# Optimization experiments

Hardware: AMD Instinct MI355X
Metric: run time of the kernel (lower is better)

## Reference

```python
import jax, jax.numpy as jnp
import numpy as np

N_USERS, N_ITEMS, N_GENRES = 31360, 6807, 18
TOTAL = N_USERS + N_ITEMS + N_GENRES          # 38185
OFFSET = TOTAL - N_GENRES                      # 38167
D = 16                                         # embedding_dim
B = 524288                                     # batch
MLP_DIMS = [64, 32, 16]
IN_DIM = 3 * D                                 # field_num * embedding_dim


def setup_inputs() -> dict:
    key = jax.random.key(0)
    ks = jax.random.split(key, 14)
    user = jax.random.randint(ks[0], (B, 1), 0, N_USERS)
    item = N_USERS + jax.random.randint(ks[1], (B, 1), 0, N_ITEMS)
    x_onehot = jnp.concatenate([user, item], axis=1)            # [B,2] global ids
    multi_hot = jax.random.randint(ks[2], (B, N_GENRES), 0, 2)  # [B,18] 0/1 mask
    s = 0.05
    emb_table = s * jax.random.normal(ks[3], (TOTAL, D), jnp.float32)
    fc_table = s * jax.random.normal(ks[4], (TOTAL, 1), jnp.float32)
    W1 = s * jax.random.normal(ks[5], (IN_DIM, MLP_DIMS[0]), jnp.float32)
    b1 = jnp.zeros((MLP_DIMS[0],), jnp.float32)
    W2 = s * jax.random.normal(ks[6], (MLP_DIMS[0], MLP_DIMS[1]), jnp.float32)
    b2 = jnp.zeros((MLP_DIMS[1],), jnp.float32)
    W3 = s * jax.random.normal(ks[7], (MLP_DIMS[1], MLP_DIMS[2]), jnp.float32)
    b3 = jnp.zeros((MLP_DIMS[2],), jnp.float32)
    W4 = s * jax.random.normal(ks[8], (MLP_DIMS[2], 1), jnp.float32)
    b4 = jnp.zeros((1,), jnp.float32)
    bias = jnp.zeros((1,), jnp.float32)
    return {"x_onehot": x_onehot, "multi_hot": multi_hot,
            "emb_table": emb_table, "fc_table": fc_table,
            "W1": W1, "b1": b1, "W2": W2, "b2": b2,
            "W3": W3, "b3": b3, "W4": W4, "b4": b4, "bias": bias}


def reference(x_onehot, multi_hot, emb_table, fc_table,
              W1, b1, W2, b2, W3, b3, W4, b4, bias):
    mh = multi_hot.astype(emb_table.dtype)                      # [B,18]
    # ragged multi-hot sum == mask @ genre slice of table (EmbeddingBag sum)
    embed_mh = mh @ emb_table[OFFSET:]                          # [B,D]
    embed_x = jnp.concatenate(
        [emb_table[x_onehot], embed_mh[:, None, :]], axis=1)    # [B,3,D]
    fc_mh = mh @ fc_table[OFFSET:]                              # [B,1]
    fc_x = jnp.concatenate(
        [fc_table[x_onehot], fc_mh[:, None, :]], axis=1)        # [B,3,1]
    # FM second-order term
    sum_e = embed_x.sum(axis=1)                                 # [B,D]
    fm_y = bias + fc_x.sum(axis=1) + 0.5 * jnp.sum(
        sum_e ** 2 - (embed_x ** 2).sum(axis=1), axis=1, keepdims=True)  # [B,1]
    # MLP (dropout inactive at inference)
    h = embed_x.reshape(embed_x.shape[0], -1)                   # [B,48]
    h = jax.nn.relu(h @ W1 + b1)
    h = jax.nn.relu(h @ W2 + b2)
    h = jax.nn.relu(h @ W3 + b3)
    mlp_y = h @ W4 + b4                                         # [B,1]
    return jax.nn.sigmoid(fm_y[:, 0] + mlp_y[:, 0])             # [B]
```

## Files before the change

### kernel.cpp

```cpp
#include <hip/hip_runtime.h>
#include <hip/hip_bf16.h>

namespace {

constexpr int kBatch  = 524288;
constexpr int kD      = 16;
constexpr int kOffset = 38167;
constexpr int kNG     = 18;

constexpr int W1B0   = 0;
constexpr int W2B0   = 8192;
constexpr int W3B0   = 12288;
constexpr int GB0    = 13312;
constexpr int WBYTES = 14336;

typedef __attribute__((ext_vector_type(8))) short short8;
typedef __attribute__((ext_vector_type(4))) float f32x4;

__device__ __forceinline__ unsigned short f2bf(float f) {
    return __builtin_bit_cast(unsigned short, __float2bfloat16(f));
}
__device__ __forceinline__ unsigned pk2(float a, float b) {
    return (unsigned)f2bf(a) | ((unsigned)f2bf(b) << 16);
}
__device__ __forceinline__ float bf2f(unsigned short s) {
    union { unsigned u; float f; } v; v.u = ((unsigned)s) << 16;
    return v.f;
}

__global__ void prep_weights(const float* __restrict__ emb,
                             const float* __restrict__ W1,
                             const float* __restrict__ W2,
                             const float* __restrict__ W3,
                             unsigned short* __restrict__ wimg)
{
    const int t = (int)threadIdx.x;
    for (int i = t; i < WBYTES / 2; i += 256) wimg[i] = 0;
    __syncthreads();
    for (int i = t; i < 48 * 64; i += 256) {
        int k = i >> 6, n = i & 63;
        int byte = W1B0 + n * 128 + ((k * 2) ^ ((n & 7) << 4));
        wimg[byte >> 1] = f2bf(W1[k * 64 + n]);
    }
    for (int i = t; i < 64 * 32; i += 256) {
        int k = i >> 5, n = i & 31;
        int byte = W2B0 + n * 128 + ((k * 2) ^ ((n & 7) << 4));
        wimg[byte >> 1] = f2bf(W2[k * 32 + n]);
    }
    for (int i = t; i < 32 * 16; i += 256) {
        int k = i >> 4, n = i & 15;
        int byte = W3B0 + n * 64 + ((k * 2) ^ ((n & 3) << 4));
        wimg[byte >> 1] = f2bf(W3[k * 16 + n]);
    }
    for (int i = t; i < 512; i += 256) {
        int c = i >> 5, r = i & 31, g = r >> 3, j = r & 7;
        int kg = 8 * g + j;
        wimg[(GB0 >> 1) + (4 * c + g) * 8 + j] =
            (kg < kNG) ? f2bf(emb[(size_t)(kOffset + kg) * kD + c]) : (unsigned short)0;
    }
}

__global__ __launch_bounds__(256, 3) void deepfm_fwd(
    const int*   __restrict__ x_onehot,
    const int*   __restrict__ multi_hot,
    const float* __restrict__ emb,
    const float* __restrict__ fc,
    const unsigned short* __restrict__ wimg,
    const float* __restrict__ b1,
    const float* __restrict__ b2,
    const float* __restrict__ b3,
    const float* __restrict__ W4,
    const float* __restrict__ b4,
    const float* __restrict__ bias,
    float*       __restrict__ out)
{
    __shared__ alignas(16) unsigned short s_w[WBYTES / 2];
    __shared__ alignas(16) unsigned short s_act[4 * 4096];

    const int t = (int)threadIdx.x;

    {
        const uint4* src = reinterpret_cast<const uint4*>(wimg);
        uint4*       dst = reinterpret_cast<uint4*>(s_w);
        #pragma unroll
        for (int q = 0; q < 4; ++q) {
            const int idx = t + 256 * q;
            if (idx < WBYTES / 16) dst[idx] = src[idx];
        }
    }

    const int i    = (int)blockIdx.x * 256 + t;
    const int lane = t & 63;
    const int w    = t >> 6;
    const int c    = lane & 15, g = lane >> 4;
    char* __restrict__ awc = (char*)(s_act + w * 4096);
    const char* __restrict__ swc = (const char*)s_w;

    const int l7 = lane & 7;
    const int sb = lane * 128;
    int rA[2];
    #pragma unroll
    for (int kt = 0; kt < 2; ++kt)
        rA[kt] = c * 128 + (((4 * kt + g) ^ (c & 7)) << 4);
    int wepi[4];
    #pragma unroll
    for (int nt = 0; nt < 4; ++nt)
        wepi[nt] = c * 128 + ((((2 * nt + (g >> 1)) ^ (c & 7))) << 4) + 8 * (g & 1);

    int2 mh[9];
    {
        const int2* mh2 = reinterpret_cast<const int2*>(multi_hot + (size_t)kNG * i);
        #pragma unroll
        for (int q = 0; q < 9; ++q) mh[q] = mh2[q];
    }
    const int2 ids = *reinterpret_cast<const int2*>(x_onehot + 2 * (size_t)i);

    float h[32];
    {
        const float4* eu = reinterpret_cast<const float4*>(emb + (size_t)ids.x * kD);
        #pragma unroll
        for (int q = 0; q < 4; ++q) {
            const float4 a = eu[q];
            h[4*q+0] = a.x; h[4*q+1] = a.y; h[4*q+2] = a.z; h[4*q+3] = a.w;
        }
        const float4* ei = reinterpret_cast<const float4*>(emb + (size_t)ids.y * kD);
        #pragma unroll
        for (int q = 0; q < 4; ++q) {
            const float4 a = ei[q];
            h[16+4*q+0] = a.x; h[16+4*q+1] = a.y; h[16+4*q+2] = a.z; h[16+4*q+3] = a.w;
        }
    }

    float4 b1q[4];
    #pragma unroll
    for (int nt = 0; nt < 4; ++nt)
        b1q[nt] = *reinterpret_cast<const float4*>(b1 + 16 * nt + 4 * g);
    float4 b2q[2];
    #pragma unroll
    for (int nt = 0; nt < 2; ++nt)
        b2q[nt] = *reinterpret_cast<const float4*>(b2 + 16 * nt + 4 * g);
    const float4 b3q = *reinterpret_cast<const float4*>(b3 + 4 * g);
    const float4 w4q = *reinterpret_cast<const float4*>(W4 + 4 * g);

    float lin = bias[0] + b4[0] + fc[ids.x] + fc[ids.y];
    #pragma unroll
    for (int q = 0; q < 9; ++q) {
        lin += mh[q].x ? fc[kOffset + 2 * q]     : 0.f;
        lin += mh[q].y ? fc[kOffset + 2 * q + 1] : 0.f;
    }

    {
        unsigned mw[9];
        #pragma unroll
        for (int q = 0; q < 9; ++q)
            mw[q] = (mh[q].x ? 0x3F80u : 0u) | (mh[q].y ? 0x3F800000u : 0u);
        uint4 v0; v0.x = mw[0]; v0.y = mw[1]; v0.z = mw[2]; v0.w = mw[3];
        uint4 v1; v1.x = mw[4]; v1.y = mw[5]; v1.z = mw[6]; v1.w = mw[7];
        uint4 v2; v2.x = mw[8]; v2.y = 0u;    v2.z = 0u;    v2.w = 0u;
        uint4 vz; vz.x = vz.y = vz.z = vz.w = 0u;
        *reinterpret_cast<uint4*>(awc + sb + ((4 ^ l7) << 4)) = v0;
        *reinterpret_cast<uint4*>(awc + sb + ((5 ^ l7) << 4)) = v1;
        *reinterpret_cast<uint4*>(awc + sb + ((6 ^ l7) << 4)) = v2;
        *reinterpret_cast<uint4*>(awc + sb + ((7 ^ l7) << 4)) = vz;
    }

    {
        #pragma unroll
        for (int q = 0; q < 4; ++q) {
            uint4 d;
            d.x = pk2(h[8*q+0], h[8*q+1]);
            d.y = pk2(h[8*q+2], h[8*q+3]);
            d.z = pk2(h[8*q+4], h[8*q+5]);
            d.w = pk2(h[8*q+6], h[8*q+7]);
            *reinterpret_cast<uint4*>(awc + sb + ((q ^ l7) << 4)) = d;
        }
    }

    float fm = 0.f;
    #pragma unroll
    for (int d = 0; d < kD; ++d) fm = fmaf(h[d], h[16 + d], fm);

    __syncthreads();

    const f32x4 z4 = {0.f, 0.f, 0.f, 0.f};

    {
        const short8 gfrag = *reinterpret_cast<const short8*>(s_w + (GB0 >> 1) + (4 * c + g) * 8);
        short8 bm[4];
        #pragma unroll
        for (int st = 0; st < 4; ++st)
            bm[st] = *reinterpret_cast<const short8*>(awc + rA[1] + 2048 * st);
        #pragma unroll
        for (int st = 0; st < 4; ++st) {
            const f32x4 accb = __builtin_amdgcn_mfma_f32_16x16x32_bf16(gfrag, bm[st], z4, 0, 0, 0);
            uint2 dv;
            dv.x = pk2(accb[0], accb[1]);
            dv.y = pk2(accb[2], accb[3]);
            *reinterpret_cast<uint2*>(awc + wepi[2] + 2048 * st) = dv;
        }
        uint4 vz; vz.x = vz.y = vz.z = vz.w = 0u;
        *reinterpret_cast<uint4*>(awc + sb + ((6 ^ l7) << 4)) = vz;
        *reinterpret_cast<uint4*>(awc + sb + ((7 ^ l7) << 4)) = vz;
    }

    {
        const uint4 p0 = *reinterpret_cast<const uint4*>(awc + sb + ((4 ^ l7) << 4));
        const uint4 p1 = *reinterpret_cast<const uint4*>(awc + sb + ((5 ^ l7) << 4));
        const unsigned pp[8] = {p0.x, p0.y, p0.z, p0.w, p1.x, p1.y, p1.z, p1.w};
        #pragma unroll
        for (int j = 0; j < 8; ++j) {
            const float e0 = bf2f((unsigned short)(pp[j] & 0xFFFFu));
            const float e1 = bf2f((unsigned short)(pp[j] >> 16));
            fm = fmaf(h[2*j]   + h[16 + 2*j],   e0, fm);
            fm = fmaf(h[2*j+1] + h[16 + 2*j+1], e1, fm);
        }
    }

    {
        short8 aW[4][2], bA[4][2];
        #pragma unroll
        for (int nt = 0; nt < 4; ++nt)
            #pragma unroll
            for (int kt = 0; kt < 2; ++kt)
                aW[nt][kt] = *reinterpret_cast<const short8*>(swc + W1B0 + rA[kt] + 2048 * nt);
        #pragma unroll
        for (int st = 0; st < 4; ++st)
            #pragma unroll
            for (int kt = 0; kt < 2; ++kt)
                bA[st][kt] = *reinterpret_cast<const short8*>(awc + rA[kt] + 2048 * st);
        #pragma unroll
        for (int st = 0; st < 4; ++st) {
            f32x4 acc[4];
            #pragma unroll
            for (int nt = 0; nt < 4; ++nt) acc[nt] = z4;
            #pragma unroll
            for (int kt = 0; kt < 2; ++kt)
                #pragma unroll
                for (int nt = 0; nt < 4; ++nt)
                    acc[nt] = __builtin_amdgcn_mfma_f32_16x16x32_bf16(aW[nt][kt], bA[st][kt], acc[nt], 0, 0, 0);
            #pragma unroll
            for (int nt = 0; nt < 4; ++nt) {
                const float v0 = fmaxf(acc[nt][0] + b1q[nt].x, 0.f);
                const float v1 = fmaxf(acc[nt][1] + b1q[nt].y, 0.f);
                const float v2 = fmaxf(acc[nt][2] + b1q[nt].z, 0.f);
                const float v3 = fmaxf(acc[nt][3] + b1q[nt].w, 0.f);
                uint2 dv; dv.x = pk2(v0, v1); dv.y = pk2(v2, v3);
                *reinterpret_cast<uint2*>(awc + wepi[nt] + 2048 * st) = dv;
            }
        }
    }

    {
        short8 aW[2][2], bA[4][2];
        #pragma unroll
        for (int nt = 0; nt < 2; ++nt)
            #pragma unroll
            for (int kt = 0; kt < 2; ++kt)
                aW[nt][kt] = *reinterpret_cast<const short8*>(swc + W2B0 + rA[kt] + 2048 * nt);
        #pragma unroll
        for (int st = 0; st < 4; ++st)
            #pragma unroll
            for (int kt = 0; kt < 2; ++kt)
                bA[st][kt] = *reinterpret_cast<const short8*>(awc + rA[kt] + 2048 * st);
        #pragma unroll
        for (int st = 0; st < 4; ++st) {
            f32x4 acc[2];
            #pragma unroll
            for (int nt = 0; nt < 2; ++nt) acc[nt] = z4;
            #pragma unroll
            for (int kt = 0; kt < 2; ++kt)
                #pragma unroll
                for (int nt = 0; nt < 2; ++nt)
                    acc[nt] = __builtin_amdgcn_mfma_f32_16x16x32_bf16(aW[nt][kt], bA[st][kt], acc[nt], 0, 0, 0);
            #pragma unroll
            for (int nt = 0; nt < 2; ++nt) {
                const float v0 = fmaxf(acc[nt][0] + b2q[nt].x, 0.f);
                const float v1 = fmaxf(acc[nt][1] + b2q[nt].y, 0.f);
                const float v2 = fmaxf(acc[nt][2] + b2q[nt].z, 0.f);
                const float v3 = fmaxf(acc[nt][3] + b2q[nt].w, 0.f);
                uint2 dv; dv.x = pk2(v0, v1); dv.y = pk2(v2, v3);
                *reinterpret_cast<uint2*>(awc + wepi[nt] + 2048 * st) = dv;
            }
        }
    }

    float tot[4];
    {
        const short8 aW = *reinterpret_cast<const short8*>(
            swc + W3B0 + c * 64 + ((g ^ (c & 3)) << 4));
        short8 bA[4];
        #pragma unroll
        for (int st = 0; st < 4; ++st)
            bA[st] = *reinterpret_cast<const short8*>(awc + rA[0] + 2048 * st);
        #pragma unroll
        for (int st = 0; st < 4; ++st) {
            const f32x4 a3 = __builtin_amdgcn_mfma_f32_16x16x32_bf16(aW, bA[st], z4, 0, 0, 0);
            float p = 0.f;
            p = fmaf(fmaxf(a3[0] + b3q.x, 0.f), w4q.x, p);
            p = fmaf(fmaxf(a3[1] + b3q.y, 0.f), w4q.y, p);
            p = fmaf(fmaxf(a3[2] + b3q.z, 0.f), w4q.z, p);
            p = fmaf(fmaxf(a3[3] + b3q.w, 0.f), w4q.w, p);
            p += __shfl_xor(p, 16, 64);
            p += __shfl_xor(p, 32, 64);
            tot[st] = p;
        }
    }
    const float m01 = (g & 1) ? tot[1] : tot[0];
    const float m23 = (g & 1) ? tot[3] : tot[2];
    const float mlp = (g & 2) ? m23 : m01;

    const float x = lin + fm + mlp;
    out[i] = 1.0f / (1.0f + __expf(-x));
}

}

extern "C" void kernel_launch(void* const* d_in, const int* in_sizes, int n_in,
                              void* d_out, int out_size, void* d_ws, size_t ws_size,
                              hipStream_t stream) {
    (void)in_sizes; (void)n_in; (void)ws_size; (void)out_size;
    const int*   x_onehot  = (const int*)  d_in[0];
    const int*   multi_hot = (const int*)  d_in[1];
    const float* emb       = (const float*)d_in[2];
    const float* fc        = (const float*)d_in[3];
    const float* W1        = (const float*)d_in[4];
    const float* b1        = (const float*)d_in[5];
    const float* W2        = (const float*)d_in[6];
    const float* b2        = (const float*)d_in[7];
    const float* W3        = (const float*)d_in[8];
    const float* b3        = (const float*)d_in[9];
    const float* W4        = (const float*)d_in[10];
    const float* b4        = (const float*)d_in[11];
    const float* biasp     = (const float*)d_in[12];
    float* out = (float*)d_out;
    unsigned short* wimg = (unsigned short*)d_ws;

    hipLaunchKernelGGL(prep_weights, dim3(1), dim3(256), 0, stream,
                       emb, W1, W2, W3, wimg);
    hipLaunchKernelGGL(deepfm_fwd, dim3(kBatch / 256), dim3(256), 0, stream,
                       x_onehot, multi_hot, emb, fc, wimg,
                       b1, b2, b3, W4, b4, biasp, out);
}
```

Baseline: 38.78 us.

## Read MLP weight fragments directly from global memory instead of staging in LDS

Drops the per-block copy of the pre-swizzled weight image into shared memory and the __syncthreads that guarded it. Each lane now loads its MFMA weight fragments and biases straight from global (L2-resident) memory, with the loads placed ahead of the stage that uses them. Shared memory per block shrinks, so the occupancy hint is raised from 3 to 4 blocks per CU. The cost is more global load traffic per wave and possibly higher register pressure from holding the fragments early.

```diff
diff --git a/kernel.cpp b/kernel.cpp
--- a/kernel.cpp
+++ b/kernel.cpp
@@ -60,7 +60,7 @@
     }
 }
 
-__global__ __launch_bounds__(256, 3) void deepfm_fwd(
+__global__ __launch_bounds__(256, 4) void deepfm_fwd(
     const int*   __restrict__ x_onehot,
     const int*   __restrict__ multi_hot,
     const float* __restrict__ emb,
@@ -74,27 +74,15 @@
     const float* __restrict__ bias,
     float*       __restrict__ out)
 {
-    __shared__ alignas(16) unsigned short s_w[WBYTES / 2];
     __shared__ alignas(16) unsigned short s_act[4 * 4096];
 
-    const int t = (int)threadIdx.x;
-
-    {
-        const uint4* src = reinterpret_cast<const uint4*>(wimg);
-        uint4*       dst = reinterpret_cast<uint4*>(s_w);
-        #pragma unroll
-        for (int q = 0; q < 4; ++q) {
-            const int idx = t + 256 * q;
-            if (idx < WBYTES / 16) dst[idx] = src[idx];
-        }
-    }
-
+    const int t    = (int)threadIdx.x;
     const int i    = (int)blockIdx.x * 256 + t;
     const int lane = t & 63;
     const int w    = t >> 6;
     const int c    = lane & 15, g = lane >> 4;
     char* __restrict__ awc = (char*)(s_act + w * 4096);
-    const char* __restrict__ swc = (const char*)s_w;
+    const char* __restrict__ wb = (const char*)wimg;
 
     const int l7 = lane & 7;
     const int sb = lane * 128;
@@ -107,13 +95,14 @@
     for (int nt = 0; nt < 4; ++nt)
         wepi[nt] = c * 128 + ((((2 * nt + (g >> 1)) ^ (c & 7))) << 4) + 8 * (g & 1);
 
+    const int2 ids = *reinterpret_cast<const int2*>(x_onehot + 2 * (size_t)i);
     int2 mh[9];
     {
         const int2* mh2 = reinterpret_cast<const int2*>(multi_hot + (size_t)kNG * i);
         #pragma unroll
         for (int q = 0; q < 9; ++q) mh[q] = mh2[q];
     }
-    const int2 ids = *reinterpret_cast<const int2*>(x_onehot + 2 * (size_t)i);
+    const short8 gfrag = *reinterpret_cast<const short8*>(wb + GB0 + (4 * c + g) * 16);
 
     float h[32];
     {
@@ -130,17 +119,6 @@
             h[16+4*q+0] = a.x; h[16+4*q+1] = a.y; h[16+4*q+2] = a.z; h[16+4*q+3] = a.w;
         }
     }
-
-    float4 b1q[4];
-    #pragma unroll
-    for (int nt = 0; nt < 4; ++nt)
-        b1q[nt] = *reinterpret_cast<const float4*>(b1 + 16 * nt + 4 * g);
-    float4 b2q[2];
-    #pragma unroll
-    for (int nt = 0; nt < 2; ++nt)
-        b2q[nt] = *reinterpret_cast<const float4*>(b2 + 16 * nt + 4 * g);
-    const float4 b3q = *reinterpret_cast<const float4*>(b3 + 4 * g);
-    const float4 w4q = *reinterpret_cast<const float4*>(W4 + 4 * g);
 
     float lin = bias[0] + b4[0] + fc[ids.x] + fc[ids.y];
     #pragma unroll
@@ -180,12 +158,9 @@
     #pragma unroll
     for (int d = 0; d < kD; ++d) fm = fmaf(h[d], h[16 + d], fm);
 
-    __syncthreads();
-
     const f32x4 z4 = {0.f, 0.f, 0.f, 0.f};
 
     {
-        const short8 gfrag = *reinterpret_cast<const short8*>(s_w + (GB0 >> 1) + (4 * c + g) * 8);
         short8 bm[4];
         #pragma unroll
         for (int st = 0; st < 4; ++st)
@@ -203,6 +178,17 @@
         *reinterpret_cast<uint4*>(awc + sb + ((7 ^ l7) << 4)) = vz;
     }
 
+    short8 aW1[4][2];
+    #pragma unroll
+    for (int nt = 0; nt < 4; ++nt)
+        #pragma unroll
+        for (int kt = 0; kt < 2; ++kt)
+            aW1[nt][kt] = *reinterpret_cast<const short8*>(wb + W1B0 + rA[kt] + 2048 * nt);
+    float4 b1q[4];
+    #pragma unroll
+    for (int nt = 0; nt < 4; ++nt)
+        b1q[nt] = *reinterpret_cast<const float4*>(b1 + 16 * nt + 4 * g);
+
     {
         const uint4 p0 = *reinterpret_cast<const uint4*>(awc + sb + ((4 ^ l7) << 4));
         const uint4 p1 = *reinterpret_cast<const uint4*>(awc + sb + ((5 ^ l7) << 4));
@@ -217,12 +203,7 @@
     }
 
     {
-        short8 aW[4][2], bA[4][2];
-        #pragma unroll
-        for (int nt = 0; nt < 4; ++nt)
-            #pragma unroll
-            for (int kt = 0; kt < 2; ++kt)
-                aW[nt][kt] = *reinterpret_cast<const short8*>(swc + W1B0 + rA[kt] + 2048 * nt);
+        short8 bA[4][2];
         #pragma unroll
         for (int st = 0; st < 4; ++st)
             #pragma unroll
@@ -237,7 +218,7 @@
             for (int kt = 0; kt < 2; ++kt)
                 #pragma unroll
                 for (int nt = 0; nt < 4; ++nt)
-                    acc[nt] = __builtin_amdgcn_mfma_f32_16x16x32_bf16(aW[nt][kt], bA[st][kt], acc[nt], 0, 0, 0);
+                    acc[nt] = __builtin_amdgcn_mfma_f32_16x16x32_bf16(aW1[nt][kt], bA[st][kt], acc[nt], 0, 0, 0);
             #pragma unroll
             for (int nt = 0; nt < 4; ++nt) {
                 const float v0 = fmaxf(acc[nt][0] + b1q[nt].x, 0.f);
@@ -250,13 +231,22 @@
         }
     }
 
-    {
-        short8 aW[2][2], bA[4][2];
-        #pragma unroll
-        for (int nt = 0; nt < 2; ++nt)
-            #pragma unroll
-            for (int kt = 0; kt < 2; ++kt)
-                aW[nt][kt] = *reinterpret_cast<const short8*>(swc + W2B0 + rA[kt] + 2048 * nt);
+    short8 aW2[2][2];
+    #pragma unroll
+    for (int nt = 0; nt < 2; ++nt)
+        #pragma unroll
+        for (int kt = 0; kt < 2; ++kt)
+            aW2[nt][kt] = *reinterpret_cast<const short8*>(wb + W2B0 + rA[kt] + 2048 * nt);
+    const short8 aW3 = *reinterpret_cast<const short8*>(wb + W3B0 + c * 64 + ((g ^ (c & 3)) << 4));
+    float4 b2q[2];
+    #pragma unroll
+    for (int nt = 0; nt < 2; ++nt)
+        b2q[nt] = *reinterpret_cast<const float4*>(b2 + 16 * nt + 4 * g);
+    const float4 b3q = *reinterpret_cast<const float4*>(b3 + 4 * g);
+    const float4 w4q = *reinterpret_cast<const float4*>(W4 + 4 * g);
+
+    {
+        short8 bA[4][2];
         #pragma unroll
         for (int st = 0; st < 4; ++st)
             #pragma unroll
@@ -271,7 +261,7 @@
             for (int kt = 0; kt < 2; ++kt)
                 #pragma unroll
                 for (int nt = 0; nt < 2; ++nt)
-                    acc[nt] = __builtin_amdgcn_mfma_f32_16x16x32_bf16(aW[nt][kt], bA[st][kt], acc[nt], 0, 0, 0);
+                    acc[nt] = __builtin_amdgcn_mfma_f32_16x16x32_bf16(aW2[nt][kt], bA[st][kt], acc[nt], 0, 0, 0);
             #pragma unroll
             for (int nt = 0; nt < 2; ++nt) {
                 const float v0 = fmaxf(acc[nt][0] + b2q[nt].x, 0.f);
@@ -286,15 +276,13 @@
 
     float tot[4];
     {
-        const short8 aW = *reinterpret_cast<const short8*>(
-            swc + W3B0 + c * 64 + ((g ^ (c & 3)) << 4));
         short8 bA[4];
         #pragma unroll
         for (int st = 0; st < 4; ++st)
             bA[st] = *reinterpret_cast<const short8*>(awc + rA[0] + 2048 * st);
         #pragma unroll
         for (int st = 0; st < 4; ++st) {
-            const f32x4 a3 = __builtin_amdgcn_mfma_f32_16x16x32_bf16(aW, bA[st], z4, 0, 0, 0);
+            const f32x4 a3 = __builtin_amdgcn_mfma_f32_16x16x32_bf16(aW3, bA[st], z4, 0, 0, 0);
             float p = 0.f;
             p = fmaf(fmaxf(a3[0] + b3q.x, 0.f), w4q.x, p);
             p = fmaf(fmaxf(a3[1] + b3q.y, 0.f), w4q.y, p);
```

Result: no change. 39.19 us (+1.1%).
